# Optimization experiments

Measured on AMD Instinct MI355X. Metric: run time of the kernel, lower is better.

## Reference

```python
import jax, jax.numpy as jnp
import numpy as np

EMBED = 1024
HEADS = 16
HEAD_DIM = EMBED // HEADS
N, SEQ = 4, 2048


def setup_inputs() -> dict:
    key = jax.random.key(0)
    ks = jax.random.split(key, 9)
    values = jax.random.normal(ks[0], (N, SEQ, EMBED), dtype=jnp.float32)
    keys = jax.random.normal(ks[1], (N, SEQ, EMBED), dtype=jnp.float32)
    query = jax.random.normal(ks[2], (N, SEQ, EMBED), dtype=jnp.float32)
    mask = jax.random.randint(ks[3], (N, 1, SEQ, SEQ), 0, 2, dtype=jnp.int32)
    s_h = 1.0 / np.sqrt(HEAD_DIM)
    s_e = 1.0 / np.sqrt(EMBED)
    Wv = jax.random.normal(ks[4], (HEAD_DIM, HEAD_DIM), dtype=jnp.float32) * s_h
    Wk = jax.random.normal(ks[5], (HEAD_DIM, HEAD_DIM), dtype=jnp.float32) * s_h
    Wq = jax.random.normal(ks[6], (HEAD_DIM, HEAD_DIM), dtype=jnp.float32) * s_h
    Wo = jax.random.normal(ks[7], (EMBED, EMBED), dtype=jnp.float32) * s_e
    bo = jax.random.normal(ks[8], (EMBED,), dtype=jnp.float32) * 0.01
    return {"values": values, "keys": keys, "query": query, "mask": mask,
            "Wv": Wv, "Wk": Wk, "Wq": Wq, "Wo": Wo, "bo": bo}


def reference(values, keys, query, mask, Wv, Wk, Wq, Wo, bo):
    n, q_len = query.shape[0], query.shape[1]
    k_len, v_len = keys.shape[1], values.shape[1]
    # split heads: [N, L, H, D]
    v = values.reshape(n, v_len, HEADS, HEAD_DIM)
    k = keys.reshape(n, k_len, HEADS, HEAD_DIM)
    q = query.reshape(n, q_len, HEADS, HEAD_DIM)
    # per-head linear projections (nn.Linear: x @ W.T)
    v = jnp.einsum('nlhd,ed->nlhe', v, Wv)
    k = jnp.einsum('nlhd,ed->nlhe', k, Wk)
    q = jnp.einsum('nlhd,ed->nlhe', q, Wq)
    # [N, H, Q, K] scores
    energy = jnp.einsum('nqhd,nkhd->nhqk', q, k)
    energy = jnp.where(mask == 0, jnp.float32(-1e20), energy)
    # note: original scales by sqrt(embed_size), not sqrt(head_dim)
    attention = jax.nn.softmax(energy / jnp.sqrt(jnp.float32(EMBED)), axis=3)
    out = jnp.einsum('nhql,nlhd->nqhd', attention, v).reshape(n, q_len, EMBED)
    return out @ Wo.T + bo
```

## Files before the change

### kernel.cpp

```cpp
#include <hip/hip_runtime.h>
#include <hip/hip_bf16.h>

typedef __attribute__((ext_vector_type(8))) short bfx8;
typedef __attribute__((ext_vector_type(4))) short bfx4;
typedef __attribute__((ext_vector_type(4))) float fx4;
typedef __attribute__((ext_vector_type(16))) float f32x16;

#define MFMA16(a,b,c) __builtin_amdgcn_mfma_f32_16x16x32_bf16((a),(b),(c),0,0,0)
#define MFMA32(a,b,c) __builtin_amdgcn_mfma_f32_32x32x16_bf16((a),(b),(c),0,0,0)

__device__ __forceinline__ f32x16 mfma32x8(bfx4 a, bfx4 b, f32x16 c){
#if __has_builtin(__builtin_amdgcn_mfma_f32_32x32x8bf16_1k)
  return __builtin_amdgcn_mfma_f32_32x32x8bf16_1k(a, b, c, 0, 0, 0);
#else
  asm("v_mfma_f32_32x32x8_bf16 %0, %1, %2, %0" : "+v"(c) : "v"(a), "v"(b));
  return c;
#endif
}

__device__ __forceinline__ unsigned short bfc(float x){
  return __builtin_bit_cast(unsigned short, __float2bfloat16(x));
}
__device__ __forceinline__ unsigned pack2(float a, float b){
  return (unsigned)bfc(a) | ((unsigned)bfc(b) << 16);
}
__device__ __forceinline__ bfx8 cvt8(const float* p){
  const float4* q = (const float4*)p;
  float4 a = q[0], b = q[1];
  bfx8 r;
  r[0]=(short)bfc(a.x); r[1]=(short)bfc(a.y); r[2]=(short)bfc(a.z); r[3]=(short)bfc(a.w);
  r[4]=(short)bfc(b.x); r[5]=(short)bfc(b.y); r[6]=(short)bfc(b.z); r[7]=(short)bfc(b.w);
  return r;
}
__device__ __forceinline__ void g2l16(const void* g, void* l){
  __builtin_amdgcn_global_load_lds((const __attribute__((address_space(1))) unsigned*)g,
                                   (__attribute__((address_space(3))) unsigned*)l, 16, 0, 0);
}
__device__ __forceinline__ float mexp(float zv, unsigned mws, int pos){
  float e = __builtin_amdgcn_exp2f(zv);
  unsigned msk = (unsigned)(((int)(mws << (31-pos))) >> 31);
  return __builtin_bit_cast(float, __builtin_bit_cast(unsigned, e) & msk);
}
__device__ __forceinline__ f32x16 zero16(){
  f32x16 z;
  #pragma unroll
  for (int i=0;i<16;++i) z[i] = 0.f;
  return z;
}

#define SCL 0.04508422002778f

__global__ __launch_bounds__(256) void prep_k(const float* __restrict__ Xv, const float* __restrict__ Xk,
                                              const float* __restrict__ Xq,
                                              const float* __restrict__ Wv, const float* __restrict__ Wk,
                                              const float* __restrict__ Wq,
                                              const int* __restrict__ M, const float* __restrict__ Wo,
                                              unsigned short* __restrict__ Vt, unsigned short* __restrict__ Kb,
                                              unsigned short* __restrict__ Qb,
                                              unsigned long long* __restrict__ mT,
                                              unsigned short* __restrict__ Wob){
  int bid = blockIdx.x;
  int tid = threadIdx.x, l = tid & 63, wv = tid >> 6, g = l >> 4, j = l & 15;
  if (bid >= 3072){
    int pid = bid - 3072;
    if (pid < 1024){
      int task = pid*4 + wv;
      int n = task >> 10, rem = task & 1023, kt = rem >> 5, qc = rem & 31;
      int qbase = qc*64;
      const int* mp = M + (size_t)n*2048*2048 + (size_t)kt*64 + l;
      unsigned long long myw = 0;
      for (int qq = 0; qq < 64; ++qq){
        unsigned long long b = __ballot(mp[(size_t)(qbase+qq)*2048] != 0);
        if (l == qq) myw = b;
      }
      mT[((size_t)n*32 + kt)*2048 + qbase + l] = myw;
    } else {
      int i = ((pid-1024)*256 + tid)*8;
      bfx8 v = cvt8(Wo + i);
      *(bfx8*)(Wob + i) = v;
    }
    return;
  }
  int which = bid >> 10;
  int r = bid & 1023;
  int nh = r >> 4, sb = r & 15;
  int n = nh >> 4, h = nh & 15;
  const float* X = (which==0) ? Xv : ((which==1) ? Xk : Xq);
  const float* W = (which==0) ? Wv : ((which==1) ? Wk : Wq);
  int s0 = sb*128 + wv*32;
  size_t xbase = (size_t)n*2048*1024 + (size_t)h*64;

  if (which){
    float sc = (which==2) ? SCL : 1.0f;
    bfx8 bw[4][2];
    for (int nt=0;nt<4;++nt) for (int ks=0;ks<2;++ks)
      bw[nt][ks] = cvt8(W + (nt*16 + j)*64 + ks*32 + g*8);
    bfx8 ax[2][2];
    for (int mt=0;mt<2;++mt){
      const float* xp = X + xbase + (size_t)(s0 + mt*16 + j)*1024;
      for (int ks=0;ks<2;++ks) ax[mt][ks] = cvt8(xp + ks*32 + g*8);
    }
    fx4 acc[2][4];
    for (int mt=0;mt<2;++mt) for (int nt=0;nt<4;++nt) acc[mt][nt] = (fx4){0.f,0.f,0.f,0.f};
    for (int mt=0;mt<2;++mt) for (int nt=0;nt<4;++nt) for (int ks=0;ks<2;++ks)
      acc[mt][nt] = MFMA16(ax[mt][ks], bw[nt][ks], acc[mt][nt]);
    unsigned short* O = ((which==1) ? Kb : Qb) + (size_t)nh*2048*64;
    for (int mt=0;mt<2;++mt) for (int nt=0;nt<4;++nt) for (int rr=0;rr<4;++rr){
      int s = s0 + mt*16 + g*4 + rr, e = nt*16 + j;
      O[(size_t)s*64 + e] = bfc(acc[mt][nt][rr]*sc);
    }
  } else {
    bfx8 aw[4][2];
    for (int mt=0;mt<4;++mt) for (int ks=0;ks<2;++ks)
      aw[mt][ks] = cvt8(W + (mt*16 + j)*64 + ks*32 + g*8);
    bfx8 bx[2][2];
    for (int nt=0;nt<2;++nt){
      const float* xp = X + xbase + (size_t)(s0 + nt*16 + j)*1024;
      for (int ks=0;ks<2;++ks) bx[nt][ks] = cvt8(xp + ks*32 + g*8);
    }
    fx4 acc[4][2];
    for (int mt=0;mt<4;++mt) for (int nt=0;nt<2;++nt) acc[mt][nt] = (fx4){0.f,0.f,0.f,0.f};
    for (int mt=0;mt<4;++mt) for (int nt=0;nt<2;++nt) for (int ks=0;ks<2;++ks)
      acc[mt][nt] = MFMA16(aw[mt][ks], bx[nt][ks], acc[mt][nt]);
    unsigned short* O = Vt + (size_t)nh*64*2048;
    for (int mt=0;mt<4;++mt) for (int nt=0;nt<2;++nt) for (int rr=0;rr<4;++rr){
      int d = mt*16 + g*4 + rr, s = s0 + nt*16 + j;
      O[(size_t)d*2048 + s] = bfc(acc[mt][nt][rr]);
    }
  }
}

__global__ __launch_bounds__(256, 4) void flash_k(const unsigned short* __restrict__ Qb,
                                                  const unsigned short* __restrict__ Kb,
                                                  const unsigned short* __restrict__ Vt,
                                                  const unsigned long long* __restrict__ mT,
                                                  unsigned short* __restrict__ AO){
  __shared__ short lK[2][64*64];
  __shared__ short lV[2][64*64];
  int tid = threadIdx.x;
  int l = tid & 63, wv = tid >> 6, hi = l >> 5, c = l & 31;
  int swc = (c & 7) ^ ((c >> 3) & 3);
  int hi4 = hi*4;
  int bid0 = blockIdx.x;
  int bid = (bid0 & 7)*128 + (bid0 >> 3);
  int nh = bid >> 4, qb = bid & 15;
  int n = nh >> 4, h = nh & 15;
  const unsigned short* Qp = Qb + (size_t)nh*131072;
  const unsigned short* Kp = Kb + (size_t)nh*131072;
  const unsigned short* Vp = Vt + (size_t)nh*131072;
  int q = qb*128 + wv*32 + c;
  bfx8 qf[4];
  #pragma unroll
  for (int s=0;s<4;++s) qf[s] = *(const bfx8*)(Qp + (size_t)q*64 + s*16 + hi*8);
  f32x16 accO0 = zero16(), accO1 = zero16();
  float ls = 0.f;
  const unsigned long long* mrow = mT + (size_t)n*65536 + q;
  int rowK0 = c*128;
  int rowK1 = rowK0 + 4096;

  int sidx0 = wv*64 + l, sidx1 = sidx0 + 256;
  int srow0 = sidx0 >> 3, scs0 = (sidx0 & 7) ^ (srow0 & 7) ^ ((srow0 >> 3) & 3);
  int srow1 = sidx1 >> 3, scs1 = (sidx1 & 7) ^ (srow1 & 7) ^ ((srow1 >> 3) & 3);
  const unsigned short* Ksrc0 = Kp + (size_t)srow0*64 + scs0*8;
  const unsigned short* Ksrc1 = Kp + (size_t)srow1*64 + scs1*8;
  const unsigned short* Vsrc0 = Vp + (size_t)srow0*2048 + scs0*8;
  const unsigned short* Vsrc1 = Vp + (size_t)srow1*2048 + scs1*8;

  #define STAGE(b, kt) do { \
    g2l16(Ksrc0 + (size_t)(kt)*4096, (char*)lK[b] + sidx0*16); \
    g2l16(Ksrc1 + (size_t)(kt)*4096, (char*)lK[b] + sidx1*16); \
    g2l16(Vsrc0 + (size_t)(kt)*64,   (char*)lV[b] + sidx0*16); \
    g2l16(Vsrc1 + (size_t)(kt)*64,   (char*)lV[b] + sidx1*16); \
  } while(0)

  STAGE(0, 0);
  __syncthreads();
  unsigned long long mwcur = mrow[0];

#define PROC_TILE(zz, mws, TT, VB) do { \
    unsigned Wt[8]; \
    _Pragma("unroll") \
    for (int wi=0; wi<8; ++wi){ \
      const int r0 = 2*wi; \
      const int pos = (r0&3) + 8*(r0>>2); \
      float p0_ = mexp((zz)[r0],   (mws), pos); \
      float p1_ = mexp((zz)[r0+1], (mws), pos+1); \
      ls += p0_ + p1_; \
      Wt[wi] = pack2(p0_, p1_); \
    } \
    _Pragma("unroll") \
    for (int wl=0; wl<4; ++wl){ \
      const int w = 4*(TT) + wl; \
      uint2 u2; u2.x = Wt[2*wl]; u2.y = Wt[2*wl+1]; \
      bfx4 pb = __builtin_bit_cast(bfx4, u2); \
      bfx4 vf0 = *(const bfx4*)((VB) + rowK0 + (((w ^ swc) << 4) + hi*8)); \
      bfx4 vf1 = *(const bfx4*)((VB) + rowK1 + (((w ^ swc) << 4) + hi*8)); \
      accO0 = mfma32x8(vf0, pb, accO0); \
      accO1 = mfma32x8(vf1, pb, accO1); \
    } \
  } while(0)

#define ATTN_ITER(BUF, NBUF, kt) do { \
    if ((kt) < 31) STAGE(NBUF, (kt)+1); \
    unsigned long long mw = mwcur; \
    mwcur = mrow[(size_t)((kt)+1 < 32 ? (kt)+1 : 31)*2048]; \
    const char* KB = (const char*)lK[BUF]; \
    const char* VB = (const char*)lV[BUF]; \
    f32x16 z0 = zero16(), z1 = zero16(); \
    _Pragma("unroll") \
    for (int s=0; s<4; ++s){ \
      bfx8 kf0 = *(const bfx8*)(KB + rowK0 + (((2*s+hi) ^ swc) << 4)); \
      bfx8 kf1 = *(const bfx8*)(KB + rowK1 + (((2*s+hi) ^ swc) << 4)); \
      z0 = MFMA32(kf0, qf[s], z0); \
      z1 = MFMA32(kf1, qf[s], z1); \
    } \
    unsigned mws0 = ((unsigned)mw) >> hi4; \
    unsigned mws1 = ((unsigned)(mw >> 32)) >> hi4; \
    PROC_TILE(z0, mws0, 0, VB); \
    PROC_TILE(z1, mws1, 1, VB); \
    __syncthreads(); \
  } while(0)

  #pragma unroll 1
  for (int kt2 = 0; kt2 < 32; kt2 += 2){
    ATTN_ITER(0, 1, kt2);
    ATTN_ITER(1, 0, kt2+1);
  }
#undef ATTN_ITER
#undef PROC_TILE
#undef STAGE

  ls += __shfl_xor(ls, 32);
  float inv = 1.0f / ls;
  unsigned short* aop = AO + ((size_t)n*2048 + q)*1024 + h*64;
  #pragma unroll
  for (int u=0; u<4; ++u){
    int d0 = u*8 + hi4;
    ushort4 o;
    o.x = bfc(accO0[4*u+0]*inv); o.y = bfc(accO0[4*u+1]*inv);
    o.z = bfc(accO0[4*u+2]*inv); o.w = bfc(accO0[4*u+3]*inv);
    *(ushort4*)(aop + d0) = o;
    ushort4 o1;
    o1.x = bfc(accO1[4*u+0]*inv); o1.y = bfc(accO1[4*u+1]*inv);
    o1.z = bfc(accO1[4*u+2]*inv); o1.w = bfc(accO1[4*u+3]*inv);
    *(ushort4*)(aop + 32 + d0) = o1;
  }
}

__global__ __launch_bounds__(256) void gemm_k(const unsigned short* __restrict__ AO,
                                              const unsigned short* __restrict__ Wob,
                                              const float* __restrict__ bo, float* __restrict__ out){
  __shared__ short lA[2][128*32], lB[2][128*32];
  int tid = threadIdx.x, l = tid & 63, wv = tid >> 6, g = l >> 4, j = l & 15;
  int wr = wv >> 1, wc = wv & 1;
  int bid = blockIdx.x;
  int m0 = (bid >> 3)*128, n0 = (bid & 7)*128;
  fx4 acc[4][4];
  #pragma unroll
  for (int mt=0;mt<4;++mt) for (int nt=0;nt<4;++nt) acc[mt][nt] = (fx4){0.f,0.f,0.f,0.f};

  int sbase = wv*128;
  int sidx0 = sbase + l, sidx1 = sbase + 64 + l;
  int srow0 = sidx0 >> 2, sc0 = sidx0 & 3;
  int srow1 = sidx1 >> 2, sc1 = sidx1 & 3;
  const unsigned short* Asrc0 = AO  + (size_t)(m0+srow0)*1024 + sc0*8;
  const unsigned short* Asrc1 = AO  + (size_t)(m0+srow1)*1024 + sc1*8;
  const unsigned short* Bsrc0 = Wob + (size_t)(n0+srow0)*1024 + sc0*8;
  const unsigned short* Bsrc1 = Wob + (size_t)(n0+srow1)*1024 + sc1*8;

  #define GSTAGE(b, kb) do { \
    g2l16(Asrc0 + (kb)*32, (char*)lA[b] + sidx0*16); \
    g2l16(Asrc1 + (kb)*32, (char*)lA[b] + sidx1*16); \
    g2l16(Bsrc0 + (kb)*32, (char*)lB[b] + sidx0*16); \
    g2l16(Bsrc1 + (kb)*32, (char*)lB[b] + sidx1*16); \
  } while(0)

  GSTAGE(0, 0);
  __syncthreads();
  int b = 0;
  for (int kb = 0; kb < 32; ++kb){
    if (kb < 31) GSTAGE(b^1, kb+1);
    bfx8 af[4], bfr[4];
    #pragma unroll
    for (int mt=0;mt<4;++mt) af[mt]  = *(const bfx8*)((const char*)lA[b] + (wr*64 + mt*16 + j)*64 + g*16);
    #pragma unroll
    for (int nt=0;nt<4;++nt) bfr[nt] = *(const bfx8*)((const char*)lB[b] + (wc*64 + nt*16 + j)*64 + g*16);
    #pragma unroll
    for (int mt=0;mt<4;++mt)
      #pragma unroll
      for (int nt=0;nt<4;++nt)
        acc[mt][nt] = MFMA16(af[mt], bfr[nt], acc[mt][nt]);
    __syncthreads();
    b ^= 1;
  }
  #undef GSTAGE

  #pragma unroll
  for (int mt=0;mt<4;++mt)
    #pragma unroll
    for (int nt=0;nt<4;++nt){
      int mm = m0 + wr*64 + mt*16 + g*4;
      int oo = n0 + wc*64 + nt*16 + j;
      float bb = bo[oo];
      #pragma unroll
      for (int rr=0;rr<4;++rr)
        out[(size_t)(mm+rr)*1024 + oo] = acc[mt][nt][rr] + bb;
    }
}

extern "C" void kernel_launch(void* const* d_in, const int* in_sizes, int n_in,
                              void* d_out, int out_size, void* d_ws, size_t ws_size,
                              hipStream_t stream){
  const float* V  = (const float*)d_in[0];
  const float* K  = (const float*)d_in[1];
  const float* Q  = (const float*)d_in[2];
  const int*   M  = (const int*)d_in[3];
  const float* Wv = (const float*)d_in[4];
  const float* Wk = (const float*)d_in[5];
  const float* Wq = (const float*)d_in[6];
  const float* Wo = (const float*)d_in[7];
  const float* bo = (const float*)d_in[8];

  char* ws = (char*)d_ws;
  unsigned short* Qb = (unsigned short*)(ws + ((size_t)0  << 20));
  unsigned short* Kb = (unsigned short*)(ws + ((size_t)16 << 20));
  unsigned short* Vt = (unsigned short*)(ws + ((size_t)32 << 20));
  unsigned short* AO = (unsigned short*)(ws + ((size_t)48 << 20));
  unsigned long long* mT = (unsigned long long*)(ws + ((size_t)64 << 20));
  unsigned short* Wob = (unsigned short*)(ws + ((size_t)66 << 20));

  hipLaunchKernelGGL(prep_k,  dim3(4608), dim3(256), 0, stream,
                     V, K, Q, Wv, Wk, Wq, M, Wo, Vt, Kb, Qb, mT, Wob);
  hipLaunchKernelGGL(flash_k, dim3(1024), dim3(256), 0, stream, Qb, Kb, Vt, mT, AO);
  hipLaunchKernelGGL(gemm_k,  dim3(512),  dim3(256), 0, stream, AO, Wob, bo, (float*)d_out);
}
```

Measured before the change: 192.1 us.

## Expand mask to per-lane bf16 pair masks and compute row sums via MFMA

Replaces the compact 64-bit transposed mask bitmap with a pre-expanded 32-bit AND mask per packed bf16 pair, laid out so each lane loads its masks with four uint4 loads per tile. The flash kernel then ANDs the packed probabilities directly instead of doing per-element shift/mask ops, and it computes the softmax denominator with an extra MFMA against a ones vector instead of scalar adds and a shuffle. This trades ALU work in the inner loop for much more mask memory traffic (a 32 MB expanded mask instead of 2 MB). It also adds an extra MFMA per PV step and launches a much larger prep grid.

```diff
diff --git a/kernel.cpp b/kernel.cpp
--- a/kernel.cpp
+++ b/kernel.cpp
@@ -36,11 +36,6 @@
   __builtin_amdgcn_global_load_lds((const __attribute__((address_space(1))) unsigned*)g,
                                    (__attribute__((address_space(3))) unsigned*)l, 16, 0, 0);
 }
-__device__ __forceinline__ float mexp(float zv, unsigned mws, int pos){
-  float e = __builtin_amdgcn_exp2f(zv);
-  unsigned msk = (unsigned)(((int)(mws << (31-pos))) >> 31);
-  return __builtin_bit_cast(float, __builtin_bit_cast(unsigned, e) & msk);
-}
 __device__ __forceinline__ f32x16 zero16(){
   f32x16 z;
   #pragma unroll
@@ -57,28 +52,24 @@
                                               const int* __restrict__ M, const float* __restrict__ Wo,
                                               unsigned short* __restrict__ Vt, unsigned short* __restrict__ Kb,
                                               unsigned short* __restrict__ Qb,
-                                              unsigned long long* __restrict__ mT,
+                                              unsigned* __restrict__ em,
                                               unsigned short* __restrict__ Wob){
   int bid = blockIdx.x;
   int tid = threadIdx.x, l = tid & 63, wv = tid >> 6, g = l >> 4, j = l & 15;
+  if (bid >= 3584){
+    unsigned t = (unsigned)(bid - 3584)*256u + (unsigned)tid;
+    int w32 = t & 31, q = (t >> 5) & 2047, kt = (t >> 16) & 31, n = t >> 21;
+    int hi = w32 >> 4, T = (w32 >> 3) & 1, wi = w32 & 7;
+    int kv = 32*T + 4*hi + 2*(wi & 1) + 8*(wi >> 1);
+    const int* src = M + ((size_t)n*2048 + q)*2048 + kt*64 + kv;
+    unsigned word = (src[0] != 0 ? 0x0000FFFFu : 0u) | (src[1] != 0 ? 0xFFFF0000u : 0u);
+    em[t] = word;
+    return;
+  }
   if (bid >= 3072){
-    int pid = bid - 3072;
-    if (pid < 1024){
-      int task = pid*4 + wv;
-      int n = task >> 10, rem = task & 1023, kt = rem >> 5, qc = rem & 31;
-      int qbase = qc*64;
-      const int* mp = M + (size_t)n*2048*2048 + (size_t)kt*64 + l;
-      unsigned long long myw = 0;
-      for (int qq = 0; qq < 64; ++qq){
-        unsigned long long b = __ballot(mp[(size_t)(qbase+qq)*2048] != 0);
-        if (l == qq) myw = b;
-      }
-      mT[((size_t)n*32 + kt)*2048 + qbase + l] = myw;
-    } else {
-      int i = ((pid-1024)*256 + tid)*8;
-      bfx8 v = cvt8(Wo + i);
-      *(bfx8*)(Wob + i) = v;
-    }
+    int i = ((bid-3072)*256 + tid)*8;
+    bfx8 v = cvt8(Wo + i);
+    *(bfx8*)(Wob + i) = v;
     return;
   }
   int which = bid >> 10;
@@ -133,14 +124,13 @@
 __global__ __launch_bounds__(256, 4) void flash_k(const unsigned short* __restrict__ Qb,
                                                   const unsigned short* __restrict__ Kb,
                                                   const unsigned short* __restrict__ Vt,
-                                                  const unsigned long long* __restrict__ mT,
+                                                  const unsigned* __restrict__ em,
                                                   unsigned short* __restrict__ AO){
   __shared__ short lK[2][64*64];
   __shared__ short lV[2][64*64];
   int tid = threadIdx.x;
   int l = tid & 63, wv = tid >> 6, hi = l >> 5, c = l & 31;
   int swc = (c & 7) ^ ((c >> 3) & 3);
-  int hi4 = hi*4;
   int bid0 = blockIdx.x;
   int bid = (bid0 & 7)*128 + (bid0 >> 3);
   int nh = bid >> 4, qb = bid & 15;
@@ -152,11 +142,13 @@
   bfx8 qf[4];
   #pragma unroll
   for (int s=0;s<4;++s) qf[s] = *(const bfx8*)(Qp + (size_t)q*64 + s*16 + hi*8);
-  f32x16 accO0 = zero16(), accO1 = zero16();
-  float ls = 0.f;
-  const unsigned long long* mrow = mT + (size_t)n*65536 + q;
+  bfx4 ones;
+  #pragma unroll
+  for (int i=0;i<4;++i) ones[i] = (short)0x3F80;
+  f32x16 accO0 = zero16(), accO1 = zero16(), acc5 = zero16();
   int rowK0 = c*128;
   int rowK1 = rowK0 + 4096;
+  const uint4* ep4 = (const uint4*)em + ((size_t)n*65536 + (size_t)q)*8 + hi*4;
 
   int sidx0 = wv*64 + l, sidx1 = sidx0 + 256;
   int srow0 = sidx0 >> 3, scs0 = (sidx0 & 7) ^ (srow0 & 7) ^ ((srow0 >> 3) & 3);
@@ -175,18 +167,15 @@
 
   STAGE(0, 0);
   __syncthreads();
-  unsigned long long mwcur = mrow[0];
-
-#define PROC_TILE(zz, mws, TT, VB) do { \
+
+#define PROC_TILE(zz, TT, VB, M0, M1) do { \
+    unsigned m8[8] = {(M0).x,(M0).y,(M0).z,(M0).w,(M1).x,(M1).y,(M1).z,(M1).w}; \
     unsigned Wt[8]; \
     _Pragma("unroll") \
     for (int wi=0; wi<8; ++wi){ \
-      const int r0 = 2*wi; \
-      const int pos = (r0&3) + 8*(r0>>2); \
-      float p0_ = mexp((zz)[r0],   (mws), pos); \
-      float p1_ = mexp((zz)[r0+1], (mws), pos+1); \
-      ls += p0_ + p1_; \
-      Wt[wi] = pack2(p0_, p1_); \
+      float p0_ = __builtin_amdgcn_exp2f((zz)[2*wi]); \
+      float p1_ = __builtin_amdgcn_exp2f((zz)[2*wi+1]); \
+      Wt[wi] = pack2(p0_, p1_) & m8[wi]; \
     } \
     _Pragma("unroll") \
     for (int wl=0; wl<4; ++wl){ \
@@ -197,13 +186,16 @@
       bfx4 vf1 = *(const bfx4*)((VB) + rowK1 + (((w ^ swc) << 4) + hi*8)); \
       accO0 = mfma32x8(vf0, pb, accO0); \
       accO1 = mfma32x8(vf1, pb, accO1); \
+      acc5  = mfma32x8(ones, pb, acc5); \
     } \
   } while(0)
 
 #define ATTN_ITER(BUF, NBUF, kt) do { \
+    uint4 mc0 = ep4[(size_t)(kt)*16384 + 0]; \
+    uint4 mc1 = ep4[(size_t)(kt)*16384 + 1]; \
+    uint4 mc2 = ep4[(size_t)(kt)*16384 + 2]; \
+    uint4 mc3 = ep4[(size_t)(kt)*16384 + 3]; \
     if ((kt) < 31) STAGE(NBUF, (kt)+1); \
-    unsigned long long mw = mwcur; \
-    mwcur = mrow[(size_t)((kt)+1 < 32 ? (kt)+1 : 31)*2048]; \
     const char* KB = (const char*)lK[BUF]; \
     const char* VB = (const char*)lV[BUF]; \
     f32x16 z0 = zero16(), z1 = zero16(); \
@@ -214,10 +206,8 @@
       z0 = MFMA32(kf0, qf[s], z0); \
       z1 = MFMA32(kf1, qf[s], z1); \
     } \
-    unsigned mws0 = ((unsigned)mw) >> hi4; \
-    unsigned mws1 = ((unsigned)(mw >> 32)) >> hi4; \
-    PROC_TILE(z0, mws0, 0, VB); \
-    PROC_TILE(z1, mws1, 1, VB); \
+    PROC_TILE(z0, 0, VB, mc0, mc1); \
+    PROC_TILE(z1, 1, VB, mc2, mc3); \
     __syncthreads(); \
   } while(0)
 
@@ -230,12 +220,11 @@
 #undef PROC_TILE
 #undef STAGE
 
-  ls += __shfl_xor(ls, 32);
-  float inv = 1.0f / ls;
+  float inv = 1.0f / acc5[0];
   unsigned short* aop = AO + ((size_t)n*2048 + q)*1024 + h*64;
   #pragma unroll
   for (int u=0; u<4; ++u){
-    int d0 = u*8 + hi4;
+    int d0 = u*8 + hi*4;
     ushort4 o;
     o.x = bfc(accO0[4*u+0]*inv); o.y = bfc(accO0[4*u+1]*inv);
     o.z = bfc(accO0[4*u+2]*inv); o.w = bfc(accO0[4*u+3]*inv);
@@ -326,11 +315,11 @@
   unsigned short* Kb = (unsigned short*)(ws + ((size_t)16 << 20));
   unsigned short* Vt = (unsigned short*)(ws + ((size_t)32 << 20));
   unsigned short* AO = (unsigned short*)(ws + ((size_t)48 << 20));
-  unsigned long long* mT = (unsigned long long*)(ws + ((size_t)64 << 20));
-  unsigned short* Wob = (unsigned short*)(ws + ((size_t)66 << 20));
-
-  hipLaunchKernelGGL(prep_k,  dim3(4608), dim3(256), 0, stream,
-                     V, K, Q, Wv, Wk, Wq, M, Wo, Vt, Kb, Qb, mT, Wob);
-  hipLaunchKernelGGL(flash_k, dim3(1024), dim3(256), 0, stream, Qb, Kb, Vt, mT, AO);
-  hipLaunchKernelGGL(gemm_k,  dim3(512),  dim3(256), 0, stream, AO, Wob, bo, (float*)d_out);
-}
+  unsigned short* Wob = (unsigned short*)(ws + ((size_t)64 << 20));
+  unsigned* em = (unsigned*)(ws + ((size_t)66 << 20));
+
+  hipLaunchKernelGGL(prep_k,  dim3(36352), dim3(256), 0, stream,
+                     V, K, Q, Wv, Wk, Wq, M, Wo, Vt, Kb, Qb, em, Wob);
+  hipLaunchKernelGGL(flash_k, dim3(1024),  dim3(256), 0, stream, Qb, Kb, Vt, em, AO);
+  hipLaunchKernelGGL(gemm_k,  dim3(512),   dim3(256), 0, stream, AO, Wob, bo, (float*)d_out);
+}
```

After: 234.1 us. +21.8%, slower.
